# Kernel optimization log

Hardware: AMD Instinct MI355X
Metric: run time of the kernel (lower is better)

Reference implementation:

```python
import jax, jax.numpy as jnp
import numpy as np
import math

B, T, D, H = 2, 2048, 1024, 16
HD = D // H


def setup_inputs() -> dict:
    key = jax.random.key(0)
    k1, k2, k3 = jax.random.split(key, 3)
    x = jax.random.normal(k1, (B, T, D), dtype=jnp.float32)
    attn_mask = jnp.ones((B, T), dtype=jnp.int32)
    W_qkv = jax.random.normal(k2, (D, 3 * D), dtype=jnp.float32) * (1.0 / math.sqrt(D))
    W_out = jax.random.normal(k3, (D, D), dtype=jnp.float32) * (1.0 / math.sqrt(D))
    return {"x": x, "attn_mask": attn_mask, "W_qkv": W_qkv, "W_out": W_out}


def reference(x, attn_mask, W_qkv, W_out):
    Bx, Tx, Dx = x.shape
    qkv = jnp.einsum("btd,de->bte", x, W_qkv)  # (B,T,3D)
    q, k, v = jnp.split(qkv, 3, axis=-1)
    # (B,T,D) -> (B,H,T,hd)
    q = q.reshape(Bx, Tx, H, HD).transpose(0, 2, 1, 3)
    k = k.reshape(Bx, Tx, H, HD).transpose(0, 2, 1, 3)
    v = v.reshape(Bx, Tx, H, HD).transpose(0, 2, 1, 3)
    scale = 1.0 / math.sqrt(HD)
    scores = jnp.einsum("bhqd,bhkd->bhqk", q, k) * scale  # (B,H,T,T)
    # padding mask over keys: (B,T) -> (B,1,1,T)
    mask = attn_mask[:, None, None, :]
    scores = jnp.where(mask == 0, jnp.float32(-jnp.inf), scores)
    attn = jax.nn.softmax(scores, axis=-1)
    out = jnp.einsum("bhqk,bhkd->bhqd", attn, v)  # (B,H,T,hd)
    out = out.transpose(0, 2, 1, 3).reshape(Bx, Tx, Dx)
    return jnp.einsum("btd,de->bte", out, W_out)
```

## Files before the change

kernel.cpp:

```cpp
#include <hip/hip_runtime.h>

#define B_ 2
#define T_ 2048
#define D_ 1024
#define H_ 16
#define HD_ 64
#define NT_ (B_*T_)

typedef __attribute__((ext_vector_type(8))) short bf16x8;
typedef __attribute__((ext_vector_type(4))) float f32x4;
typedef __attribute__((ext_vector_type(16))) float f32x16;
typedef __attribute__((ext_vector_type(4))) int i32x4;

#define MFMA32(a, b, c) __builtin_amdgcn_mfma_f32_32x32x16_bf16((a), (b), (c), 0, 0, 0)

static __device__ __forceinline__ unsigned short f2bf(float f) {
    union { float f; unsigned u; } v; v.f = f;
    unsigned r = v.u + 0x7fffu + ((v.u >> 16) & 1u);
    return (unsigned short)(r >> 16);
}

static __device__ __forceinline__ float exp2a(float x) {
    float r; asm("v_exp_f32 %0, %1" : "=v"(r) : "v"(x)); return r;
}

static __device__ __forceinline__ unsigned cvt_pk_bf16(float lo, float hi) {
    unsigned r; asm("v_cvt_pk_bf16_f32 %0, %1, %2" : "=v"(r) : "v"(lo), "v"(hi)); return r;
}

static __device__ __forceinline__ void gload_lds16(const unsigned short* g, unsigned short* l) {
    __builtin_amdgcn_global_load_lds(
        (const __attribute__((address_space(1))) unsigned int*)g,
        (__attribute__((address_space(3))) unsigned int*)l, 16, 0, 0);
}

__global__ __launch_bounds__(256) void cast_f32_bf16(
    const float* __restrict__ in, unsigned short* __restrict__ out, int n) {
    int base = (blockIdx.x * blockDim.x + threadIdx.x) * 8;
    if (base >= n) return;
    f32x4 a = *(const f32x4*)(in + base);
    f32x4 b = *(const f32x4*)(in + base + 4);
    unsigned short o[8];
#pragma unroll
    for (int j = 0; j < 4; ++j) { o[j] = f2bf(a[j]); o[j + 4] = f2bf(b[j]); }
    *(i32x4*)(out + base) = *(const i32x4*)o;
}

__global__ __launch_bounds__(256) void transpose_cast(
    const float* __restrict__ in, unsigned short* __restrict__ out, int R, int C) {
    __shared__ float tile[32][33];
    int c0 = blockIdx.x * 32, r0 = blockIdx.y * 32;
    int tx = threadIdx.x, ty = threadIdx.y;
#pragma unroll
    for (int j = 0; j < 32; j += 8)
        tile[ty + j][tx] = in[(size_t)(r0 + ty + j) * C + c0 + tx];
    __syncthreads();
#pragma unroll
    for (int j = 0; j < 32; j += 8)
        out[(size_t)(c0 + ty + j) * R + r0 + tx] = f2bf(tile[tx][ty + j]);
}

template <int EPI>
__global__ __launch_bounds__(256) void gemm_bt(
    const unsigned short* __restrict__ A, const unsigned short* __restrict__ Bt,
    float* __restrict__ C,
    unsigned short* __restrict__ Qo, unsigned short* __restrict__ Ko,
    unsigned short* __restrict__ Vo,
    int M, int N, int K) {
    __shared__ __align__(16) unsigned short As[128 * 32];
    __shared__ __align__(16) unsigned short Bs[128 * 32];
    int tid = threadIdx.x;
    int wv = tid >> 6, lane = tid & 63;
    int wr = wv >> 1, wc = wv & 1;
    int l15 = lane & 15, lg = lane >> 4;
    int tm = blockIdx.y * 128, tn = blockIdx.x * 128;
    f32x4 acc[4][4] = {};

    int lrow = lane >> 2, lcol = (lane & 3) * 8;

    for (int kt = 0; kt < K; kt += 32) {
        __syncthreads();
#pragma unroll
        for (int c = 0; c < 2; ++c) {
            int chunk = wv + c * 4;
            gload_lds16(A + (size_t)(tm + chunk * 16 + lrow) * K + kt + lcol, As + chunk * 512);
            gload_lds16(Bt + (size_t)(tn + chunk * 16 + lrow) * K + kt + lcol, Bs + chunk * 512);
        }
        __syncthreads();
        bf16x8 af[4], bfr[4];
#pragma unroll
        for (int m = 0; m < 4; ++m)
            af[m] = *(const bf16x8*)(As + (wr * 64 + m * 16 + l15) * 32 + lg * 8);
#pragma unroll
        for (int n = 0; n < 4; ++n)
            bfr[n] = *(const bf16x8*)(Bs + (wc * 64 + n * 16 + l15) * 32 + lg * 8);
#pragma unroll
        for (int m = 0; m < 4; ++m)
#pragma unroll
            for (int n = 0; n < 4; ++n)
                acc[m][n] = __builtin_amdgcn_mfma_f32_16x16x32_bf16(af[m], bfr[n], acc[m][n], 0, 0, 0);
    }

    if (EPI == 0) {
#pragma unroll
        for (int m = 0; m < 4; ++m) {
            int row0 = tm + wr * 64 + m * 16 + lg * 4;
#pragma unroll
            for (int n = 0; n < 4; ++n) {
                int col = tn + wc * 64 + n * 16 + l15;
#pragma unroll
                for (int r = 0; r < 4; ++r)
                    C[(size_t)(row0 + r) * N + col] = acc[m][n][r];
            }
        }
    } else {
        const float SC = 0.125f * 1.44269504f;
#pragma unroll
        for (int m = 0; m < 4; ++m) {
            int row0 = tm + wr * 64 + m * 16 + lg * 4;
#pragma unroll
            for (int n = 0; n < 4; ++n) {
                int e = tn + wc * 64 + n * 16 + l15;
                int sec = e >> 10, rem = e & 1023;
                int h = rem >> 6, hd = rem & 63;
                int tok = row0;
                int b = tok >> 11, tl = tok & 2047;
                if (sec == 2) {
                    size_t idx0 = ((size_t)(b * H_ + h) * HD_ + hd) * T_ + tl;
                    *(unsigned*)(Vo + idx0)     = cvt_pk_bf16(acc[m][n][0], acc[m][n][1]);
                    *(unsigned*)(Vo + idx0 + 2) = cvt_pk_bf16(acc[m][n][2], acc[m][n][3]);
                } else {
                    unsigned short* dst = (sec == 0) ? Qo : Ko;
                    float sc = (sec == 0) ? SC : 1.0f;
#pragma unroll
                    for (int r = 0; r < 4; ++r)
                        dst[(((size_t)(b * H_ + h) * T_ + tl + r) << 6) + hd] =
                            f2bf(acc[m][n][r] * sc);
                }
            }
        }
    }
}

#define KPAD 72
#define VPAD 136

#define EXCH(PV, HF, FRAG)                                                     \
  do {                                                                         \
    unsigned uA0 = cvt_pk_bf16(PV[8 * HF + 0], PV[8 * HF + 1]);                \
    unsigned uA1 = cvt_pk_bf16(PV[8 * HF + 2], PV[8 * HF + 3]);                \
    unsigned uB0 = cvt_pk_bf16(PV[8 * HF + 4], PV[8 * HF + 5]);                \
    unsigned uB1 = cvt_pk_bf16(PV[8 * HF + 6], PV[8 * HF + 7]);                \
    unsigned snd0 = hi ? uA0 : uB0, snd1 = hi ? uA1 : uB1;                     \
    unsigned rc0 = (unsigned)__shfl_xor((int)snd0, 32);                        \
    unsigned rc1 = (unsigned)__shfl_xor((int)snd1, 32);                        \
    union { bf16x8 v; unsigned u[4]; } Fx;                                     \
    Fx.u[0] = hi ? rc0 : uA0;                                                  \
    Fx.u[1] = hi ? rc1 : uA1;                                                  \
    Fx.u[2] = hi ? uB0 : rc0;                                                  \
    Fx.u[3] = hi ? uB1 : rc1;                                                  \
    FRAG = Fx.v;                                                               \
  } while (0)

__global__ __launch_bounds__(256) void flash_attn(
    const unsigned short* __restrict__ Qg, const unsigned short* __restrict__ Kg,
    const unsigned short* __restrict__ VTg, const int* __restrict__ mask,
    unsigned short* __restrict__ AO) {
    __shared__ __align__(16) unsigned short Ks[128 * KPAD];
    __shared__ __align__(16) unsigned short VTs[64 * VPAD];
    __shared__ float biasS[128];

    int tid = threadIdx.x, wv = tid >> 6, lane = tid & 63;
    int l31 = lane & 31, hi = lane >> 5;
    int bh = blockIdx.y;
    int b = bh >> 4, h = bh & 15;
    int q0 = blockIdx.x * 128;
    const unsigned short* Qb  = Qg  + (size_t)bh * T_ * HD_;
    const unsigned short* Kb  = Kg  + (size_t)bh * T_ * HD_;
    const unsigned short* VTb = VTg + (size_t)bh * HD_ * T_;

    bf16x8 qf[4];
    {
        const unsigned short* qrow = Qb + (size_t)(q0 + wv * 32 + l31) * HD_;
#pragma unroll
        for (int c = 0; c < 4; ++c)
            qf[c] = *(const bf16x8*)(qrow + c * 16 + hi * 8);
    }

    float l_part = 0.f;
    f32x16 o0 = {}, o1 = {};

    i32x4 kv[4], vvv[4];
#pragma unroll
    for (int c = 0; c < 4; ++c) {
        int idx = tid + c * 256;
        kv[c]  = *(const i32x4*)(Kb + (size_t)(idx >> 3) * HD_ + (idx & 7) * 8);
        vvv[c] = *(const i32x4*)(VTb + (size_t)(idx >> 4) * T_ + (idx & 15) * 8);
    }
    int mA = mask[b * T_ + lane];
    int mB = mask[b * T_ + 64 + lane];

    for (int kt = 0; kt < T_; kt += 128) {
        bool nomask = __all(mA != 0 && mB != 0);
        __syncthreads();
#pragma unroll
        for (int c = 0; c < 4; ++c) {
            int idx = tid + c * 256;
            *(i32x4*)(Ks + (idx >> 3) * KPAD + (idx & 7) * 8) = kv[c];
            *(i32x4*)(VTs + (idx >> 4) * VPAD + (idx & 15) * 8) = vvv[c];
        }
        if (!nomask && wv == 0) {
            biasS[lane]      = mA ? 0.f : -1e30f;
            biasS[64 + lane] = mB ? 0.f : -1e30f;
        }
        if (kt + 128 < T_) {
#pragma unroll
            for (int c = 0; c < 4; ++c) {
                int idx = tid + c * 256;
                kv[c]  = *(const i32x4*)(Kb + (size_t)(kt + 128 + (idx >> 3)) * HD_ + (idx & 7) * 8);
                vvv[c] = *(const i32x4*)(VTb + (size_t)(idx >> 4) * T_ + kt + 128 + (idx & 15) * 8);
            }
            mA = mask[b * T_ + kt + 128 + lane];
            mB = mask[b * T_ + kt + 192 + lane];
        }
        __syncthreads();

#pragma unroll
        for (int hp = 0; hp < 2; ++hp) {
            f32x16 s0 = {}, s1 = {};
            __builtin_amdgcn_s_setprio(1);
#pragma unroll
            for (int c = 0; c < 4; ++c) {
                bf16x8 ka = *(const bf16x8*)(Ks + ((hp * 2 + 0) * 32 + l31) * KPAD + c * 16 + hi * 8);
                s0 = MFMA32(ka, qf[c], s0);
            }
#pragma unroll
            for (int c = 0; c < 4; ++c) {
                bf16x8 kb2 = *(const bf16x8*)(Ks + ((hp * 2 + 1) * 32 + l31) * KPAD + c * 16 + hi * 8);
                s1 = MFMA32(kb2, qf[c], s1);
            }
            __builtin_amdgcn_s_setprio(0);

            if (!nomask) {
#pragma unroll
                for (int i = 0; i < 16; ++i) {
                    int krow = (i & 3) + 8 * (i >> 2) + 4 * hi;
                    s0[i] += biasS[hp * 64 + krow];
                    s1[i] += biasS[hp * 64 + 32 + krow];
                }
            }
#pragma unroll
            for (int i = 0; i < 16; ++i) {
                s0[i] = exp2a(s0[i]);
                s1[i] = exp2a(s1[i]);
                l_part += s0[i] + s1[i];
            }
            bf16x8 fr0, fr1, fr2, fr3;
            EXCH(s0, 0, fr0);
            EXCH(s0, 1, fr1);
            EXCH(s1, 0, fr2);
            EXCH(s1, 1, fr3);

            __builtin_amdgcn_s_setprio(1);
#pragma unroll
            for (int kc = 0; kc < 4; ++kc) {
                bf16x8 fr = (kc == 0) ? fr0 : (kc == 1) ? fr1 : (kc == 2) ? fr2 : fr3;
                bf16x8 va = *(const bf16x8*)(VTs + l31 * VPAD + hp * 64 + kc * 16 + hi * 8);
                bf16x8 vb = *(const bf16x8*)(VTs + (32 + l31) * VPAD + hp * 64 + kc * 16 + hi * 8);
                o0 = MFMA32(fr, va, o0);
                o1 = MFMA32(fr, vb, o1);
            }
            __builtin_amdgcn_s_setprio(0);
        }
    }

    l_part += __shfl_xor(l_part, 32);

    size_t rowD = (size_t)(b * T_ + q0 + wv * 32) * D_ + h * 64;
#pragma unroll
    for (int i = 0; i < 16; ++i) {
        int qrow = (i & 3) + 8 * (i >> 2) + 4 * hi;
        float lq = __shfl(l_part, qrow);
        float inv = 1.0f / lq;
        AO[rowD + (size_t)qrow * D_ + l31]      = f2bf(o0[i] * inv);
        AO[rowD + (size_t)qrow * D_ + 32 + l31] = f2bf(o1[i] * inv);
    }
}

extern "C" void kernel_launch(void* const* d_in, const int* in_sizes, int n_in,
                              void* d_out, int out_size, void* d_ws, size_t ws_size,
                              hipStream_t stream) {
    const float* x    = (const float*)d_in[0];
    const int*   mask = (const int*)d_in[1];
    const float* Wqkv = (const float*)d_in[2];
    const float* Wout = (const float*)d_in[3];
    float* out = (float*)d_out;
    char* ws = (char*)d_ws;

    unsigned short* Xb    = (unsigned short*)(ws);
    unsigned short* WqkvT = (unsigned short*)(ws + (size_t)(8u << 20));
    unsigned short* WoutT = (unsigned short*)(ws + (size_t)(14u << 20));
    unsigned short* Qg    = (unsigned short*)(ws + (size_t)(16u << 20));
    unsigned short* Kg    = (unsigned short*)(ws + (size_t)(24u << 20));
    unsigned short* VT    = (unsigned short*)(ws + (size_t)(32u << 20));
    unsigned short* AO    = Xb;

    cast_f32_bf16<<<2048, 256, 0, stream>>>(x, Xb, NT_ * D_);
    transpose_cast<<<dim3(3072 / 32, 1024 / 32), dim3(32, 8), 0, stream>>>(Wqkv, WqkvT, 1024, 3072);
    transpose_cast<<<dim3(1024 / 32, 1024 / 32), dim3(32, 8), 0, stream>>>(Wout, WoutT, 1024, 1024);
    gemm_bt<1><<<dim3(3072 / 128, 4096 / 128), 256, 0, stream>>>(
        Xb, WqkvT, nullptr, Qg, Kg, VT, NT_, 3 * D_, D_);
    flash_attn<<<dim3(T_ / 128, B_ * H_), 256, 0, stream>>>(Qg, Kg, VT, mask, AO);
    gemm_bt<0><<<dim3(1024 / 128, 4096 / 128), 256, 0, stream>>>(
        AO, WoutT, out, nullptr, nullptr, nullptr, NT_, D_, D_);
}
```

Measured before the change: 137.0 us.

## Split attention KV range across two wave groups and swizzle blocks across XCDs

The flash attention block grows to 512 threads. Two groups of four waves each handle half of a 256-key tile, and their partial outputs and row sums are combined through shared memory at the end. The goal is more waves in flight per query tile, which hides load and exp latency. Separately, an XCD-aware block index swizzle is applied to the GEMMs and attention so that neighbouring tiles land on the same chiplet and share L2. The cost is larger LDS use, an extra reduction pass, and possibly lower occupancy.

```diff
diff --git a/kernel.cpp b/kernel.cpp
--- a/kernel.cpp
+++ b/kernel.cpp
@@ -32,6 +32,14 @@
     __builtin_amdgcn_global_load_lds(
         (const __attribute__((address_space(1))) unsigned int*)g,
         (__attribute__((address_space(3))) unsigned int*)l, 16, 0, 0);
+}
+
+static __device__ __forceinline__ void xcd_swz(int& bx, int& by) {
+    int gx = gridDim.x, nwg = gx * gridDim.y;
+    int flat = by * gx + bx;
+    int cpx = nwg >> 3;
+    int swz = (flat & 7) * cpx + (flat >> 3);
+    bx = swz % gx; by = swz / gx;
 }
 
 __global__ __launch_bounds__(256) void cast_f32_bf16(
@@ -73,7 +81,9 @@
     int wv = tid >> 6, lane = tid & 63;
     int wr = wv >> 1, wc = wv & 1;
     int l15 = lane & 15, lg = lane >> 4;
-    int tm = blockIdx.y * 128, tn = blockIdx.x * 128;
+    int bx = blockIdx.x, by = blockIdx.y;
+    xcd_swz(bx, by);
+    int tm = by * 128, tn = bx * 128;
     f32x4 acc[4][4] = {};
 
     int lrow = lane >> 2, lcol = (lane & 3) * 8;
@@ -143,7 +153,9 @@
 }
 
 #define KPAD 72
-#define VPAD 136
+#define VPAD2 264
+#define KS_BYTES (256 * KPAD * 2)
+#define VT_BYTES (64 * VPAD2 * 2)
 
 #define EXCH(PV, HF, FRAG)                                                     \
   do {                                                                         \
@@ -162,26 +174,32 @@
     FRAG = Fx.v;                                                               \
   } while (0)
 
-__global__ __launch_bounds__(256) void flash_attn(
+__global__ __launch_bounds__(512, 4) void flash_attn(
     const unsigned short* __restrict__ Qg, const unsigned short* __restrict__ Kg,
     const unsigned short* __restrict__ VTg, const int* __restrict__ mask,
     unsigned short* __restrict__ AO) {
-    __shared__ __align__(16) unsigned short Ks[128 * KPAD];
-    __shared__ __align__(16) unsigned short VTs[64 * VPAD];
-    __shared__ float biasS[128];
+    __shared__ __align__(16) char smem[KS_BYTES + VT_BYTES + 256 * 4];
+    unsigned short* Ks  = (unsigned short*)smem;
+    unsigned short* VTs = (unsigned short*)(smem + KS_BYTES);
+    float* biasS        = (float*)(smem + KS_BYTES + VT_BYTES);
+    float* redO         = (float*)smem;
+    float* redL         = (float*)(smem + 256 * 34 * 4);
 
     int tid = threadIdx.x, wv = tid >> 6, lane = tid & 63;
     int l31 = lane & 31, hi = lane >> 5;
-    int bh = blockIdx.y;
+    int wg = wv >> 2, wq = wv & 3;
+    int bx = blockIdx.x, by = blockIdx.y;
+    xcd_swz(bx, by);
+    int bh = by;
     int b = bh >> 4, h = bh & 15;
-    int q0 = blockIdx.x * 128;
+    int q0 = bx * 128;
     const unsigned short* Qb  = Qg  + (size_t)bh * T_ * HD_;
     const unsigned short* Kb  = Kg  + (size_t)bh * T_ * HD_;
     const unsigned short* VTb = VTg + (size_t)bh * HD_ * T_;
 
     bf16x8 qf[4];
     {
-        const unsigned short* qrow = Qb + (size_t)(q0 + wv * 32 + l31) * HD_;
+        const unsigned short* qrow = Qb + (size_t)(q0 + wq * 32 + l31) * HD_;
 #pragma unroll
         for (int c = 0; c < 4; ++c)
             qf[c] = *(const bf16x8*)(qrow + c * 16 + hi * 8);
@@ -193,35 +211,32 @@
     i32x4 kv[4], vvv[4];
 #pragma unroll
     for (int c = 0; c < 4; ++c) {
-        int idx = tid + c * 256;
+        int idx = tid + c * 512;
         kv[c]  = *(const i32x4*)(Kb + (size_t)(idx >> 3) * HD_ + (idx & 7) * 8);
-        vvv[c] = *(const i32x4*)(VTb + (size_t)(idx >> 4) * T_ + (idx & 15) * 8);
-    }
-    int mA = mask[b * T_ + lane];
-    int mB = mask[b * T_ + 64 + lane];
-
-    for (int kt = 0; kt < T_; kt += 128) {
+        vvv[c] = *(const i32x4*)(VTb + (size_t)(idx >> 5) * T_ + (idx & 31) * 8);
+    }
+    int mA = mask[b * T_ + wg * 128 + lane];
+    int mB = mask[b * T_ + wg * 128 + 64 + lane];
+
+    for (int kt2 = 0; kt2 < T_; kt2 += 256) {
         bool nomask = __all(mA != 0 && mB != 0);
         __syncthreads();
 #pragma unroll
         for (int c = 0; c < 4; ++c) {
-            int idx = tid + c * 256;
+            int idx = tid + c * 512;
             *(i32x4*)(Ks + (idx >> 3) * KPAD + (idx & 7) * 8) = kv[c];
-            *(i32x4*)(VTs + (idx >> 4) * VPAD + (idx & 15) * 8) = vvv[c];
-        }
-        if (!nomask && wv == 0) {
-            biasS[lane]      = mA ? 0.f : -1e30f;
-            biasS[64 + lane] = mB ? 0.f : -1e30f;
-        }
-        if (kt + 128 < T_) {
+            *(i32x4*)(VTs + (idx >> 5) * VPAD2 + (idx & 31) * 8) = vvv[c];
+        }
+        if (tid < 256) biasS[tid] = (mask[b * T_ + kt2 + tid] != 0) ? 0.f : -1e30f;
+        if (kt2 + 256 < T_) {
 #pragma unroll
             for (int c = 0; c < 4; ++c) {
-                int idx = tid + c * 256;
-                kv[c]  = *(const i32x4*)(Kb + (size_t)(kt + 128 + (idx >> 3)) * HD_ + (idx & 7) * 8);
-                vvv[c] = *(const i32x4*)(VTb + (size_t)(idx >> 4) * T_ + kt + 128 + (idx & 15) * 8);
-            }
-            mA = mask[b * T_ + kt + 128 + lane];
-            mB = mask[b * T_ + kt + 192 + lane];
+                int idx = tid + c * 512;
+                kv[c]  = *(const i32x4*)(Kb + (size_t)(kt2 + 256 + (idx >> 3)) * HD_ + (idx & 7) * 8);
+                vvv[c] = *(const i32x4*)(VTb + (size_t)(idx >> 5) * T_ + kt2 + 256 + (idx & 31) * 8);
+            }
+            mA = mask[b * T_ + kt2 + 256 + wg * 128 + lane];
+            mB = mask[b * T_ + kt2 + 256 + wg * 128 + 64 + lane];
         }
         __syncthreads();
 
@@ -231,12 +246,12 @@
             __builtin_amdgcn_s_setprio(1);
 #pragma unroll
             for (int c = 0; c < 4; ++c) {
-                bf16x8 ka = *(const bf16x8*)(Ks + ((hp * 2 + 0) * 32 + l31) * KPAD + c * 16 + hi * 8);
+                bf16x8 ka = *(const bf16x8*)(Ks + (wg * 128 + hp * 64 + l31) * KPAD + c * 16 + hi * 8);
                 s0 = MFMA32(ka, qf[c], s0);
             }
 #pragma unroll
             for (int c = 0; c < 4; ++c) {
-                bf16x8 kb2 = *(const bf16x8*)(Ks + ((hp * 2 + 1) * 32 + l31) * KPAD + c * 16 + hi * 8);
+                bf16x8 kb2 = *(const bf16x8*)(Ks + (wg * 128 + hp * 64 + 32 + l31) * KPAD + c * 16 + hi * 8);
                 s1 = MFMA32(kb2, qf[c], s1);
             }
             __builtin_amdgcn_s_setprio(0);
@@ -245,8 +260,8 @@
 #pragma unroll
                 for (int i = 0; i < 16; ++i) {
                     int krow = (i & 3) + 8 * (i >> 2) + 4 * hi;
-                    s0[i] += biasS[hp * 64 + krow];
-                    s1[i] += biasS[hp * 64 + 32 + krow];
+                    s0[i] += biasS[wg * 128 + hp * 64 + krow];
+                    s1[i] += biasS[wg * 128 + hp * 64 + 32 + krow];
                 }
             }
 #pragma unroll
@@ -265,8 +280,8 @@
 #pragma unroll
             for (int kc = 0; kc < 4; ++kc) {
                 bf16x8 fr = (kc == 0) ? fr0 : (kc == 1) ? fr1 : (kc == 2) ? fr2 : fr3;
-                bf16x8 va = *(const bf16x8*)(VTs + l31 * VPAD + hp * 64 + kc * 16 + hi * 8);
-                bf16x8 vb = *(const bf16x8*)(VTs + (32 + l31) * VPAD + hp * 64 + kc * 16 + hi * 8);
+                bf16x8 va = *(const bf16x8*)(VTs + l31 * VPAD2 + wg * 128 + hp * 64 + kc * 16 + hi * 8);
+                bf16x8 vb = *(const bf16x8*)(VTs + (32 + l31) * VPAD2 + wg * 128 + hp * 64 + kc * 16 + hi * 8);
                 o0 = MFMA32(fr, va, o0);
                 o1 = MFMA32(fr, vb, o1);
             }
@@ -276,7 +291,24 @@
 
     l_part += __shfl_xor(l_part, 32);
 
-    size_t rowD = (size_t)(b * T_ + q0 + wv * 32) * D_ + h * 64;
+    __syncthreads();
+    if (wg == 1) {
+        float* dst = redO + (wq * 64 + lane) * 34;
+#pragma unroll
+        for (int i = 0; i < 16; ++i) { dst[i] = o0[i]; dst[16 + i] = o1[i]; }
+        redL[wq * 64 + lane] = l_part;
+    }
+    __syncthreads();
+    if (wg == 1) return;
+
+    {
+        const float* src = redO + (wq * 64 + lane) * 34;
+#pragma unroll
+        for (int i = 0; i < 16; ++i) { o0[i] += src[i]; o1[i] += src[16 + i]; }
+        l_part += redL[wq * 64 + lane];
+    }
+
+    size_t rowD = (size_t)(b * T_ + q0 + wq * 32) * D_ + h * 64;
 #pragma unroll
     for (int i = 0; i < 16; ++i) {
         int qrow = (i & 3) + 8 * (i >> 2) + 4 * hi;
@@ -310,7 +342,7 @@
     transpose_cast<<<dim3(1024 / 32, 1024 / 32), dim3(32, 8), 0, stream>>>(Wout, WoutT, 1024, 1024);
     gemm_bt<1><<<dim3(3072 / 128, 4096 / 128), 256, 0, stream>>>(
         Xb, WqkvT, nullptr, Qg, Kg, VT, NT_, 3 * D_, D_);
-    flash_attn<<<dim3(T_ / 128, B_ * H_), 256, 0, stream>>>(Qg, Kg, VT, mask, AO);
+    flash_attn<<<dim3(T_ / 128, B_ * H_), 512, 0, stream>>>(Qg, Kg, VT, mask, AO);
     gemm_bt<0><<<dim3(1024 / 128, 4096 / 128), 256, 0, stream>>>(
         AO, WoutT, out, nullptr, nullptr, nullptr, NT_, D_, D_);
 }
```

New measurement: 254.2 us. 85.6% more time.
